# Kernel optimization log

Measured on AMD Instinct MI355X. Metric: run time of the kernel, lower is better.

The kernel has to match this reference:

```python
import jax, jax.numpy as jnp
import numpy as np

B_, C_, H_, W_ = 8, 512, 64, 64

def conv1x1(x, W, b):
    # 1x1 conv == per-pixel linear: [B,C,H,W] x [O,C] -> [B,O,H,W]
    return jnp.einsum('bchw,oc->bohw', x, W) + b[None, :, None, None]

def setup_inputs() -> dict:
    key = jax.random.key(0)
    ks = jax.random.split(key, 7)
    s = 1.0 / np.sqrt(C_)
    return {
        'x': jax.random.normal(ks[0], (B_, C_, H_, W_), dtype=jnp.float32),
        'wA': jax.random.normal(ks[1], (C_, C_), dtype=jnp.float32) * s,
        'bA': jax.random.normal(ks[2], (C_,), dtype=jnp.float32) * s,
        'wB': jax.random.normal(ks[3], (C_, C_), dtype=jnp.float32) * s,
        'bB': jax.random.normal(ks[4], (C_,), dtype=jnp.float32) * s,
        'wV': jax.random.normal(ks[5], (C_, C_), dtype=jnp.float32) * s,
        'bV': jax.random.normal(ks[6], (C_,), dtype=jnp.float32) * s,
    }

def reference(x, wA, bA, wB, bB, wV, bV):
    b, c, h, w = x.shape
    hw = h * w
    A = conv1x1(x, wA, bA).reshape(b, c, hw)                      # feature maps
    Bm = jax.nn.softmax(conv1x1(x, wB, bB).reshape(b, c, hw), axis=-1)  # attention maps
    # global_descriptors[b,i,j] = mean_hw softmax(B)[b,i,hw] * A[b,j,hw]
    # == fused softmax + batched matmul, avoiding the O(C*C*HW) broadcast.
    gd = jnp.einsum('bik,bjk->bij', Bm, A) / hw                    # [b, c, c]
    av = jax.nn.softmax(conv1x1(x, wV, bV).reshape(b, c, hw), axis=-1)
    # out[b,j,hw] = sum_i av[b,i,hw] * gd[b,i,j]
    out = jnp.einsum('bih,bij->bjh', av, gd)                       # [b, c, hw]
    return out.reshape(b, c, h, w)
```

## Files before the change

kernel.cpp:

```cpp
#include <hip/hip_runtime.h>
#include <math.h>

#define BB 8
#define CC 512
#define HWN 4096

typedef __bf16 bf16x8 __attribute__((ext_vector_type(8)));
typedef __bf16 bf16x4 __attribute__((ext_vector_type(4)));
typedef float f32x4 __attribute__((ext_vector_type(4)));

#define GLOBAL_AS __attribute__((address_space(1)))
#define LDS_AS __attribute__((address_space(3)))

static __device__ __forceinline__ void async_copy16(const void* g, void* l) {
  __builtin_amdgcn_global_load_lds((const GLOBAL_AS unsigned int*)g,
                                   (LDS_AS unsigned int*)l, 16, 0, 0);
}

template <int BIASMODE, typename OUT_T>
__global__ __launch_bounds__(256) void gemm_mfma_bt(
    const __bf16* __restrict__ Ag, const __bf16* __restrict__ Bg,
    const float* __restrict__ bias, OUT_T* __restrict__ Cg,
    int M, int N, int K, long sA, long sB, long sC, float alpha,
    int ksl, long sSlice) {
  __shared__ __bf16 As[128][32];
  __shared__ __bf16 Bs[128][32];

  const int tid = threadIdx.x;
  const int n0 = blockIdx.x * 128;
  const int m0 = blockIdx.y * 128;
  const int bz = blockIdx.z;
  const int batch = bz / ksl;
  const int slice = bz - batch * ksl;
  const int kLen = K / ksl;
  const int kBeg = slice * kLen, kEnd = kBeg + kLen;
  Ag += (long)batch * sA;
  Bg += (long)batch * sB;
  Cg += (long)batch * sC + (long)slice * sSlice;

  const int lane = tid & 63;
  const int w = tid >> 6;
  const int wr = w >> 1;
  const int wc = w & 1;
  const int l15 = lane & 15;
  const int quad = lane >> 4;

  const int srow = w * 16 + (lane >> 2);
  const int scol = (lane & 3) * 8;

  f32x4 acc[4][4] = {};

  for (int k0 = kBeg; k0 < kEnd; k0 += 32) {
    __syncthreads();
#pragma unroll
    for (int i = 0; i < 2; i++) {
      async_copy16(&Ag[(long)(m0 + i * 64 + srow) * K + k0 + scol],
                   (char*)&As[0][0] + i * 4096 + w * 1024);
      async_copy16(&Bg[(long)(n0 + i * 64 + srow) * K + k0 + scol],
                   (char*)&Bs[0][0] + i * 4096 + w * 1024);
    }
    __syncthreads();

    bf16x8 af[4], bfr[4];
#pragma unroll
    for (int t = 0; t < 4; t++) {
      af[t]  = *(const bf16x8*)&As[wr * 64 + t * 16 + l15][quad * 8];
      bfr[t] = *(const bf16x8*)&Bs[wc * 64 + t * 16 + l15][quad * 8];
    }
#pragma unroll
    for (int ti = 0; ti < 4; ti++)
#pragma unroll
      for (int tj = 0; tj < 4; tj++)
        acc[ti][tj] = __builtin_amdgcn_mfma_f32_16x16x32_bf16(
            af[ti], bfr[tj], acc[ti][tj], 0, 0, 0);
  }

#pragma unroll
  for (int ti = 0; ti < 4; ti++) {
#pragma unroll
    for (int tj = 0; tj < 4; tj++) {
#pragma unroll
      for (int r = 0; r < 4; r++) {
        const int m = m0 + wr * 64 + ti * 16 + quad * 4 + r;
        const int n = n0 + wc * 64 + tj * 16 + l15;
        float v = acc[ti][tj][r];
        if (BIASMODE == 1) v += bias[m];
        Cg[(long)m * N + n] = (OUT_T)(v * alpha);
      }
    }
  }
}

__global__ __launch_bounds__(256) void softmax_dual_bf16(
    __bf16* __restrict__ logits, __bf16* __restrict__ bm) {
  const int row = blockIdx.x;
  const int b = row >> 10, c = row & 1023;
  __bf16* src = logits + ((long)b * 1024 + c) * HWN;
  __bf16* dst = (c < 512) ? (bm + ((long)b * 512 + c) * HWN) : src;
  const int tid = threadIdx.x;

  const bf16x8* p = reinterpret_cast<const bf16x8*>(src);
  bf16x8* q = reinterpret_cast<bf16x8*>(dst);

  float v[16];
  float vmax = -3.0e38f;
#pragma unroll
  for (int i = 0; i < 2; i++) {
    bf16x8 t = p[tid + i * 256];
#pragma unroll
    for (int j = 0; j < 8; j++) {
      v[i * 8 + j] = (float)t[j];
      vmax = fmaxf(vmax, v[i * 8 + j]);
    }
  }
#pragma unroll
  for (int off = 32; off > 0; off >>= 1)
    vmax = fmaxf(vmax, __shfl_xor(vmax, off, 64));

  __shared__ float red[4];
  const int wid = tid >> 6;
  if ((tid & 63) == 0) red[wid] = vmax;
  __syncthreads();
  vmax = fmaxf(fmaxf(red[0], red[1]), fmaxf(red[2], red[3]));
  __syncthreads();

  float s = 0.f;
#pragma unroll
  for (int i = 0; i < 16; i++) {
    v[i] = expf(v[i] - vmax);
    s += v[i];
  }
#pragma unroll
  for (int off = 32; off > 0; off >>= 1) s += __shfl_xor(s, off, 64);
  if ((tid & 63) == 0) red[wid] = s;
  __syncthreads();
  s = (red[0] + red[1]) + (red[2] + red[3]);

  const float inv = 1.0f / s;
#pragma unroll
  for (int i = 0; i < 2; i++) {
    bf16x8 o;
#pragma unroll
    for (int j = 0; j < 8; j++) o[j] = (__bf16)(v[i * 8 + j] * inv);
    q[tid + i * 256] = o;
  }
}

__global__ __launch_bounds__(256) void reduce_partials8(
    const float* __restrict__ P, __bf16* __restrict__ out, long sBat,
    long sSl) {
  const int b = blockIdx.x >> 8;
  const int il = ((blockIdx.x & 255) * 256 + threadIdx.x) * 4;
  const float* p = P + (long)b * sBat + il;
  float4 s0 = *(const float4*)&p[0];
#pragma unroll
  for (int sl = 1; sl < 8; sl++) {
    float4 t = *(const float4*)&p[sl * sSl];
    s0.x += t.x; s0.y += t.y; s0.z += t.z; s0.w += t.w;
  }
  bf16x4 o;
  o[0] = (__bf16)s0.x; o[1] = (__bf16)s0.y; o[2] = (__bf16)s0.z;
  o[3] = (__bf16)s0.w;
  *(bf16x4*)&out[(long)b * 262144 + il] = o;
}

__global__ __launch_bounds__(256) void convert_x(
    const float* __restrict__ x, __bf16* __restrict__ xb,
    __bf16* __restrict__ xT) {
  __shared__ __bf16 t[64][66];
  const int j0 = blockIdx.x * 64;
  const int c0 = blockIdx.y * 64;
  const long bofs = (long)blockIdx.z * CC * HWN;
  const int j = threadIdx.x & 63;
  const int g = threadIdx.x >> 6;

#pragma unroll
  for (int r = 0; r < 16; r++) {
    const int i = r * 4 + g;
    const float v = x[bofs + (long)(c0 + i) * HWN + j0 + j];
    const __bf16 bv = (__bf16)v;
    xb[bofs + (long)(c0 + i) * HWN + j0 + j] = bv;
    t[j][i] = bv;
  }
  __syncthreads();
#pragma unroll
  for (int r = 0; r < 16; r++) {
    const int jj = r * 4 + g;
    xT[bofs + (long)(j0 + jj) * CC + c0 + j] = t[jj][j];
  }
}

__global__ __launch_bounds__(256) void transpose_bf16_s(
    const __bf16* __restrict__ in, __bf16* __restrict__ out, int ldIn,
    long sIn, long sOut) {
  __shared__ __bf16 t[64][66];
  const int j0 = blockIdx.x * 64;
  const int c0 = blockIdx.y * 64;
  const int j = threadIdx.x & 63;
  const int g = threadIdx.x >> 6;

#pragma unroll
  for (int r = 0; r < 16; r++) {
    const int i = r * 4 + g;
    t[j][i] = in[(long)blockIdx.z * sIn + (long)(c0 + i) * ldIn + j0 + j];
  }
  __syncthreads();
#pragma unroll
  for (int r = 0; r < 16; r++) {
    const int jj = r * 4 + g;
    out[(long)blockIdx.z * sOut + (long)(j0 + jj) * CC + c0 + j] = t[jj][j];
  }
}

__global__ __launch_bounds__(256) void cast_weights(
    const float* __restrict__ wA, const float* __restrict__ wB,
    const float* __restrict__ wV, const float* __restrict__ bB,
    const float* __restrict__ bV, __bf16* __restrict__ wAb,
    __bf16* __restrict__ wBVb, float* __restrict__ bBV) {
  if (blockIdx.x == 768) {
#pragma unroll
    for (int j = 0; j < 4; j++) {
      const int i = threadIdx.x * 4 + j;
      bBV[i] = (i < 512) ? bB[i] : bV[i - 512];
    }
    return;
  }
  const int which = blockIdx.x >> 8;
  const int i = ((blockIdx.x & 255) * 256 + threadIdx.x) * 4;
  const float* in = which == 0 ? wB : (which == 1 ? wV : wA);
  __bf16* out = which == 0 ? wBVb
                           : (which == 1 ? wBVb + 262144 : wAb);
  float4 v = *(const float4*)&in[i];
  bf16x4 o;
  o[0] = (__bf16)v.x; o[1] = (__bf16)v.y; o[2] = (__bf16)v.z;
  o[3] = (__bf16)v.w;
  *(bf16x4*)&out[i] = o;
}

extern "C" void kernel_launch(void* const* d_in, const int* in_sizes, int n_in,
                              void* d_out, int out_size, void* d_ws,
                              size_t ws_size, hipStream_t stream) {
  const float* x  = (const float*)d_in[0];
  const float* wA = (const float*)d_in[1];
  const float* bA = (const float*)d_in[2];
  const float* wB = (const float*)d_in[3];
  const float* bB = (const float*)d_in[4];
  const float* wV = (const float*)d_in[5];
  const float* bV = (const float*)d_in[6];
  float* out = (float*)d_out;

  const size_t nBCHW = (size_t)BB * CC * HWN;
  const size_t nBCC  = (size_t)BB * CC * CC;
  __bf16* xb   = (__bf16*)d_ws;
  __bf16* xT   = xb + nBCHW;
  __bf16* bm   = xT + nBCHW;
  __bf16* Mb   = bm + nBCHW;
  __bf16* gdT  = Mb + nBCC;
  __bf16* wBVb = gdT + nBCC;
  __bf16* wAb  = wBVb + (size_t)1024 * CC;
  float*  bBV  = (float*)(wAb + (size_t)CC * CC);

  const long sBC_HW = (long)CC * HWN;
  const long sCC = (long)CC * CC;

  cast_weights<<<dim3(769), 256, 0, stream>>>(wA, wB, wV, bB, bV, wAb, wBVb,
                                              bBV);
  convert_x<<<dim3(HWN / 64, CC / 64, BB), 256, 0, stream>>>(x, xb, xT);

  __bf16* logits = (__bf16*)d_out;

  gemm_mfma_bt<1, __bf16><<<dim3(HWN / 128, 1024 / 128, BB), 256, 0, stream>>>(
      wBVb, xT, bBV, logits, 1024, HWN, CC, 0, sBC_HW, (long)1024 * HWN, 1.0f,
      1, 0);
  softmax_dual_bf16<<<dim3(BB * 1024), 256, 0, stream>>>(logits, bm);
  transpose_bf16_s<<<dim3(HWN / 64, CC / 64, BB), 256, 0, stream>>>(
      logits + 2097152, xT, HWN, (long)1024 * HWN, (long)HWN * CC);
  gemm_mfma_bt<0, float><<<dim3(CC / 128, CC / 128, BB * 8), 256, 0, stream>>>(
      bm, xb, nullptr, out, CC, CC, HWN, sBC_HW, sBC_HW, (long)2097152, 1.0f,
      8, (long)262144);
  reduce_partials8<<<dim3(BB * 256), 256, 0, stream>>>(out, Mb, 2097152,
                                                       262144);
  gemm_mfma_bt<1, __bf16><<<dim3(CC / 128, CC / 128, BB), 256, 0, stream>>>(
      wAb, Mb, bA, gdT, CC, CC, CC, 0, sCC, sCC, 1.0f / (float)HWN, 1, 0);
  gemm_mfma_bt<0, float><<<dim3(HWN / 128, CC / 128, BB), 256, 0, stream>>>(
      gdT, xT, nullptr, out, CC, HWN, CC, sCC, sBC_HW, sBC_HW, 1.0f, 1, 0);
}
```

Measured before the change: 320.5 us.

## Double K-tile per GEMM iteration, store split-K partials in bf16, fuse conversion kernels

The MFMA GEMM now loads a 64-wide K slab per barrier pair (two 32-wide halves in LDS), halving synchronisation count. Split-K partial sums for the Bm·A GEMM are written as bf16 instead of fp32, and the reduction kernel reads bf16x8 vectors. The weight cast and x conversion/transposition kernels are merged into a single launch. Storing partials in bf16 reduces memory traffic but adds rounding error before accumulation.

```diff
diff --git a/kernel.cpp b/kernel.cpp
--- a/kernel.cpp
+++ b/kernel.cpp
@@ -23,8 +23,8 @@
     const float* __restrict__ bias, OUT_T* __restrict__ Cg,
     int M, int N, int K, long sA, long sB, long sC, float alpha,
     int ksl, long sSlice) {
-  __shared__ __bf16 As[128][32];
-  __shared__ __bf16 Bs[128][32];
+  __shared__ __bf16 As[2][128][32];
+  __shared__ __bf16 Bs[2][128][32];
 
   const int tid = threadIdx.x;
   const int n0 = blockIdx.x * 128;
@@ -40,39 +40,43 @@
 
   const int lane = tid & 63;
   const int w = tid >> 6;
-  const int wr = w >> 1;
-  const int wc = w & 1;
-  const int l15 = lane & 15;
-  const int quad = lane >> 4;
-
-  const int srow = w * 16 + (lane >> 2);
+  const int wr = w >> 1, wc = w & 1;
+  const int l15 = lane & 15, quad = lane >> 4;
+
+  const int srow = w * 32 + (lane >> 2);
   const int scol = (lane & 3) * 8;
 
   f32x4 acc[4][4] = {};
 
-  for (int k0 = kBeg; k0 < kEnd; k0 += 32) {
+  for (int k0 = kBeg; k0 < kEnd; k0 += 64) {
     __syncthreads();
 #pragma unroll
-    for (int i = 0; i < 2; i++) {
-      async_copy16(&Ag[(long)(m0 + i * 64 + srow) * K + k0 + scol],
-                   (char*)&As[0][0] + i * 4096 + w * 1024);
-      async_copy16(&Bg[(long)(n0 + i * 64 + srow) * K + k0 + scol],
-                   (char*)&Bs[0][0] + i * 4096 + w * 1024);
+    for (int h = 0; h < 2; h++) {
+#pragma unroll
+      for (int j = 0; j < 2; j++) {
+        async_copy16(&Ag[(long)(m0 + srow + j * 16) * K + k0 + h * 32 + scol],
+                     (char*)&As[h][0][0] + w * 2048 + j * 1024);
+        async_copy16(&Bg[(long)(n0 + srow + j * 16) * K + k0 + h * 32 + scol],
+                     (char*)&Bs[h][0][0] + w * 2048 + j * 1024);
+      }
     }
     __syncthreads();
 
-    bf16x8 af[4], bfr[4];
-#pragma unroll
-    for (int t = 0; t < 4; t++) {
-      af[t]  = *(const bf16x8*)&As[wr * 64 + t * 16 + l15][quad * 8];
-      bfr[t] = *(const bf16x8*)&Bs[wc * 64 + t * 16 + l15][quad * 8];
-    }
-#pragma unroll
-    for (int ti = 0; ti < 4; ti++)
-#pragma unroll
-      for (int tj = 0; tj < 4; tj++)
-        acc[ti][tj] = __builtin_amdgcn_mfma_f32_16x16x32_bf16(
-            af[ti], bfr[tj], acc[ti][tj], 0, 0, 0);
+#pragma unroll
+    for (int h = 0; h < 2; h++) {
+      bf16x8 af[4], bfr[4];
+#pragma unroll
+      for (int t = 0; t < 4; t++) {
+        af[t]  = *(const bf16x8*)&As[h][wr * 64 + t * 16 + l15][quad * 8];
+        bfr[t] = *(const bf16x8*)&Bs[h][wc * 64 + t * 16 + l15][quad * 8];
+      }
+#pragma unroll
+      for (int ti = 0; ti < 4; ti++)
+#pragma unroll
+        for (int tj = 0; tj < 4; tj++)
+          acc[ti][tj] = __builtin_amdgcn_mfma_f32_16x16x32_bf16(
+              af[ti], bfr[tj], acc[ti][tj], 0, 0, 0);
+    }
   }
 
 #pragma unroll
@@ -146,27 +150,59 @@
   }
 }
 
-__global__ __launch_bounds__(256) void reduce_partials8(
-    const float* __restrict__ P, __bf16* __restrict__ out, long sBat,
-    long sSl) {
-  const int b = blockIdx.x >> 8;
-  const int il = ((blockIdx.x & 255) * 256 + threadIdx.x) * 4;
-  const float* p = P + (long)b * sBat + il;
-  float4 s0 = *(const float4*)&p[0];
-#pragma unroll
-  for (int sl = 1; sl < 8; sl++) {
-    float4 t = *(const float4*)&p[sl * sSl];
-    s0.x += t.x; s0.y += t.y; s0.z += t.z; s0.w += t.w;
-  }
-  bf16x4 o;
-  o[0] = (__bf16)s0.x; o[1] = (__bf16)s0.y; o[2] = (__bf16)s0.z;
-  o[3] = (__bf16)s0.w;
-  *(bf16x4*)&out[(long)b * 262144 + il] = o;
-}
-
-__global__ __launch_bounds__(256) void convert_x(
+__global__ __launch_bounds__(256) void reduce_partials8b(
+    const __bf16* __restrict__ P, __bf16* __restrict__ out) {
+  const long i = ((long)blockIdx.x * 256 + threadIdx.x) * 8;
+  const int b = (int)(i >> 18);
+  const long il = i & 262143;
+  const __bf16* p = P + (long)b * 2097152 + il;
+  float s[8] = {};
+#pragma unroll
+  for (int sl = 0; sl < 8; sl++) {
+    bf16x8 t = *(const bf16x8*)&p[(long)sl * 262144];
+#pragma unroll
+    for (int j = 0; j < 8; j++) s[j] += (float)t[j];
+  }
+  bf16x8 o;
+#pragma unroll
+  for (int j = 0; j < 8; j++) o[j] = (__bf16)s[j];
+  *(bf16x8*)&out[i] = o;
+}
+
+__global__ __launch_bounds__(256) void convert_all(
     const float* __restrict__ x, __bf16* __restrict__ xb,
-    __bf16* __restrict__ xT) {
+    __bf16* __restrict__ xT, const float* __restrict__ wA,
+    const float* __restrict__ wB, const float* __restrict__ wV,
+    const float* __restrict__ bB, const float* __restrict__ bV,
+    __bf16* __restrict__ wAb, __bf16* __restrict__ wBVb,
+    float* __restrict__ bBV) {
+  if (blockIdx.z == 8) {
+    const int t = blockIdx.y * 64 + blockIdx.x;
+    const int grp = t >> 7;
+    const int r = t & 127;
+    if (grp == 3) {
+      if (r == 0) {
+#pragma unroll
+        for (int j = 0; j < 4; j++) {
+          const int i = threadIdx.x * 4 + j;
+          bBV[i] = (i < 512) ? bB[i] : bV[i - 512];
+        }
+      }
+      return;
+    }
+    const float* in = grp == 0 ? wB : (grp == 1 ? wV : wA);
+    __bf16* o = grp == 0 ? wBVb : (grp == 1 ? wBVb + 262144 : wAb);
+    const long base = (long)r * 2048 + threadIdx.x * 8;
+    float4 v0 = *(const float4*)&in[base];
+    float4 v1 = *(const float4*)&in[base + 4];
+    bf16x8 ob;
+    ob[0] = (__bf16)v0.x; ob[1] = (__bf16)v0.y; ob[2] = (__bf16)v0.z;
+    ob[3] = (__bf16)v0.w; ob[4] = (__bf16)v1.x; ob[5] = (__bf16)v1.y;
+    ob[6] = (__bf16)v1.z; ob[7] = (__bf16)v1.w;
+    *(bf16x8*)&o[base] = ob;
+    return;
+  }
+
   __shared__ __bf16 t[64][66];
   const int j0 = blockIdx.x * 64;
   const int c0 = blockIdx.y * 64;
@@ -210,31 +246,6 @@
     const int jj = r * 4 + g;
     out[(long)blockIdx.z * sOut + (long)(j0 + jj) * CC + c0 + j] = t[jj][j];
   }
-}
-
-__global__ __launch_bounds__(256) void cast_weights(
-    const float* __restrict__ wA, const float* __restrict__ wB,
-    const float* __restrict__ wV, const float* __restrict__ bB,
-    const float* __restrict__ bV, __bf16* __restrict__ wAb,
-    __bf16* __restrict__ wBVb, float* __restrict__ bBV) {
-  if (blockIdx.x == 768) {
-#pragma unroll
-    for (int j = 0; j < 4; j++) {
-      const int i = threadIdx.x * 4 + j;
-      bBV[i] = (i < 512) ? bB[i] : bV[i - 512];
-    }
-    return;
-  }
-  const int which = blockIdx.x >> 8;
-  const int i = ((blockIdx.x & 255) * 256 + threadIdx.x) * 4;
-  const float* in = which == 0 ? wB : (which == 1 ? wV : wA);
-  __bf16* out = which == 0 ? wBVb
-                           : (which == 1 ? wBVb + 262144 : wAb);
-  float4 v = *(const float4*)&in[i];
-  bf16x4 o;
-  o[0] = (__bf16)v.x; o[1] = (__bf16)v.y; o[2] = (__bf16)v.z;
-  o[3] = (__bf16)v.w;
-  *(bf16x4*)&out[i] = o;
 }
 
 extern "C" void kernel_launch(void* const* d_in, const int* in_sizes, int n_in,
@@ -263,9 +274,8 @@
   const long sBC_HW = (long)CC * HWN;
   const long sCC = (long)CC * CC;
 
-  cast_weights<<<dim3(769), 256, 0, stream>>>(wA, wB, wV, bB, bV, wAb, wBVb,
-                                              bBV);
-  convert_x<<<dim3(HWN / 64, CC / 64, BB), 256, 0, stream>>>(x, xb, xT);
+  convert_all<<<dim3(HWN / 64, CC / 64, BB + 1), 256, 0, stream>>>(
+      x, xb, xT, wA, wB, wV, bB, bV, wAb, wBVb, bBV);
 
   __bf16* logits = (__bf16*)d_out;
 
@@ -275,11 +285,11 @@
   softmax_dual_bf16<<<dim3(BB * 1024), 256, 0, stream>>>(logits, bm);
   transpose_bf16_s<<<dim3(HWN / 64, CC / 64, BB), 256, 0, stream>>>(
       logits + 2097152, xT, HWN, (long)1024 * HWN, (long)HWN * CC);
-  gemm_mfma_bt<0, float><<<dim3(CC / 128, CC / 128, BB * 8), 256, 0, stream>>>(
-      bm, xb, nullptr, out, CC, CC, HWN, sBC_HW, sBC_HW, (long)2097152, 1.0f,
-      8, (long)262144);
-  reduce_partials8<<<dim3(BB * 256), 256, 0, stream>>>(out, Mb, 2097152,
-                                                       262144);
+  gemm_mfma_bt<0, __bf16><<<dim3(CC / 128, CC / 128, BB * 8), 256, 0,
+                            stream>>>(bm, xb, nullptr, (__bf16*)out, CC, CC,
+                                      HWN, sBC_HW, sBC_HW, (long)2097152,
+                                      1.0f, 8, (long)262144);
+  reduce_partials8b<<<dim3(1024), 256, 0, stream>>>((const __bf16*)out, Mb);
   gemm_mfma_bt<1, __bf16><<<dim3(CC / 128, CC / 128, BB), 256, 0, stream>>>(
       wAb, Mb, bA, gdT, CC, CC, CC, 0, sCC, sCC, 1.0f / (float)HWN, 1, 0);
   gemm_mfma_bt<0, float><<<dim3(HWN / 128, CC / 128, BB), 256, 0, stream>>>(
```

Measured after the change: 295.5 us. 7.8% less time.
